# Performance work log

Hardware: AMD Instinct MI355X
Metric: run time of the kernel (lower is better)

Reference implementation:

```python
import jax, jax.numpy as jnp
import numpy as np
from itertools import combinations_with_replacement

KSIZE = 13  # 1 + 6*int(start_scale) with start_scale=2.0 (fixed at init)


def gaussian_kernel3d(scale):
    # torch: sigma = max(0.1, min(sigma, 10)); kernel detached (requires_grad=False)
    sigma = jnp.clip(jax.lax.stop_gradient(scale), 0.1, 10.0)
    k1 = jnp.arange(KSIZE, dtype=jnp.float32) - KSIZE // 2
    k1 = jnp.exp(-(k1 ** 2) / (2.0 * sigma ** 2))
    k3 = jnp.einsum('i,j,k->ijk', k1, k1, k1)
    return k3 / k3.sum()


def blur3d(vol, kernel):
    # replicate ('edge') padding then VALID conv, matching padding_mode='replicate'
    p = KSIZE // 2
    vp = jnp.pad(vol, ((0, 0), (0, 0), (p, p), (p, p), (p, p)), mode='edge')
    w = kernel[None, None]  # [O=1, I=1, kD, kH, kW]
    return jax.lax.conv_general_dilated(
        vp, w, window_strides=(1, 1, 1), padding='VALID',
        dimension_numbers=('NCDHW', 'OIDHW', 'NCDHW'))


def tgrad(f, axis):
    # torch.gradient: central diff interior, one-sided first-order at edges
    n = f.shape[axis]
    sl = lambda a, b: jax.lax.slice_in_dim(f, a, b, axis=axis)
    interior = (sl(2, n) - sl(0, n - 2)) * 0.5
    first = sl(1, 2) - sl(0, 1)
    last = sl(n - 1, n) - sl(n - 2, n - 1)
    return jnp.concatenate([first, interior, last], axis=axis)


def setup_inputs() -> dict:
    key = jax.random.key(0)
    kx, k1, k2, k3, k4 = jax.random.split(key, 5)
    B, D, H, W = 2, 128, 128, 128
    x = jax.random.normal(kx, (B, 1, D, H, W), dtype=jnp.float32)
    scale = jnp.asarray(2.0, dtype=jnp.float32)
    # Linear(7,10) and Linear(10,1), torch layout [out, in]
    lim1 = 1.0 / np.sqrt(7.0)
    lim2 = 1.0 / np.sqrt(10.0)
    W1 = jax.random.uniform(k1, (10, 7), jnp.float32, -lim1, lim1)
    b1 = jax.random.uniform(k2, (10,), jnp.float32, -lim1, lim1)
    W2 = jax.random.uniform(k3, (1, 10), jnp.float32, -lim2, lim2)
    b2 = jax.random.uniform(k4, (1,), jnp.float32, -lim2, lim2)
    return {'x': x, 'scale': scale, 'W1': W1, 'b1': b1, 'W2': W2, 'b2': b2}


def reference(x, scale, W1, b1, W2, b2):
    B = x.shape[0]
    D, H, W = x.shape[2], x.shape[3], x.shape[4]
    smoothed = blur3d(x, gaussian_kernel3d(scale))  # [B,1,D,H,W]
    axes = [2, 3, 4]
    g = [tgrad(smoothed, a) for a in axes]
    H_elems = [tgrad(g[a0 - 2], a1) for a0, a1 in combinations_with_replacement(axes, 2)]
    h = jnp.stack(H_elems)                      # [6,B,1,D,H,W]
    h = jnp.moveaxis(h, 0, -1)                  # [B,1,D,H,W,6]
    h = h.reshape(B, D * H * W, 6)              # flatten dims 1..4 (C=1)
    scale_col = jnp.broadcast_to(scale, (B, D * H * W, 1))
    feat = jnp.concatenate([h, scale_col], axis=2)  # [B,N,7]
    hid = jax.nn.relu(feat @ W1.T + b1)             # [B,N,10]
    out = jax.nn.sigmoid(hid @ W2.T + b2)           # [B,N,1]
    out = out.reshape(B, D, H, W, 1)
    return jnp.transpose(out, (0, 4, 1, 2, 3))      # [B,1,D,H,W]
```

## Files before the change

### kernel.cpp

```cpp
#include <hip/hip_runtime.h>
#include <math.h>

#define NVOX (2 * 128 * 128 * 128)
#define KS 13
#define KR 6
#define LROWS 44

__device__ __forceinline__ float4 LD4(const float* p) {
    return *reinterpret_cast<const float4*>(p);
}

__device__ __forceinline__ void make_weights(float scale, float* wv) {
    float sig = fminf(fmaxf(scale, 0.1f), 10.0f);
    float inv2s2 = -1.0f / (2.0f * sig * sig);
    float sum = 0.f;
#pragma unroll
    for (int t = 0; t < KS; ++t) {
        float d = (float)(t - KR);
        wv[t] = __expf(d * d * inv2s2);
        sum += wv[t];
    }
    float r = 1.0f / sum;
#pragma unroll
    for (int t = 0; t < KS; ++t) wv[t] *= r;
}

__global__ __launch_bounds__(256) void wh_blur_kernel(const float* __restrict__ in,
                                                      float* __restrict__ out,
                                                      const float* __restrict__ scale_p) {
    __shared__ float T[LROWS * 128];
    const int i = blockIdx.x;
    const int wid = ((i & 7) << 7) | (i >> 3);
    const int slice = wid >> 2;
    const int h0 = (wid & 3) << 5;
    const float* sp = in + (slice << 14);
    float* op = out + (slice << 14);

    float wv[KS];
    make_weights(scale_p[0], wv);

    for (int it = 0; it < 3; ++it) {
        int g = threadIdx.x + (it << 8);
        if (g < LROWS * 16) {
            int wseg = g & 15;
            int w0 = wseg << 3;
            int lr = g >> 4;
            int r = h0 - 6 + lr;
            r = r < 0 ? 0 : (r > 127 ? 127 : r);
            const float* rp = sp + (r << 7);

            float F[24];
            if (wseg >= 1 && wseg <= 14) {
#pragma unroll
                for (int i2 = 0; i2 < 6; ++i2) {
                    float4 q = LD4(rp + w0 - 8 + (i2 << 2));
                    F[4 * i2] = q.x; F[4 * i2 + 1] = q.y;
                    F[4 * i2 + 2] = q.z; F[4 * i2 + 3] = q.w;
                }
            } else if (wseg == 0) {
                float e = rp[0];
#pragma unroll
                for (int i2 = 0; i2 < 8; ++i2) F[i2] = e;
#pragma unroll
                for (int i2 = 0; i2 < 4; ++i2) {
                    float4 q = LD4(rp + (i2 << 2));
                    F[8 + 4 * i2] = q.x; F[9 + 4 * i2] = q.y;
                    F[10 + 4 * i2] = q.z; F[11 + 4 * i2] = q.w;
                }
            } else {
                float e = rp[127];
#pragma unroll
                for (int i2 = 0; i2 < 4; ++i2) {
                    float4 q = LD4(rp + 112 + (i2 << 2));
                    F[4 * i2] = q.x; F[4 * i2 + 1] = q.y;
                    F[4 * i2 + 2] = q.z; F[4 * i2 + 3] = q.w;
                }
#pragma unroll
                for (int i2 = 16; i2 < 24; ++i2) F[i2] = e;
            }

            float a[8];
#pragma unroll
            for (int k = 0; k < 8; ++k) a[k] = 0.f;
#pragma unroll
            for (int t = 0; t < KS; ++t) {
                float wt = wv[t];
#pragma unroll
                for (int k = 0; k < 8; ++k) a[k] = fmaf(wt, F[k + 2 + t], a[k]);
            }
            *reinterpret_cast<float4*>(&T[(lr << 7) + w0]) =
                make_float4(a[0], a[1], a[2], a[3]);
            *reinterpret_cast<float4*>(&T[(lr << 7) + w0 + 4]) =
                make_float4(a[4], a[5], a[6], a[7]);
        }
    }
    __syncthreads();

    {
        const int w0 = (threadIdx.x & 31) << 2;
        const int r0 = (threadIdx.x >> 5) << 2;

        float4 win[KS];
#pragma unroll
        for (int t = 0; t < KS; ++t) win[t] = LD4(&T[((r0 + t) << 7) + w0]);
#pragma unroll
        for (int s = 0; s < 4; ++s) {
            float4 acc = make_float4(0.f, 0.f, 0.f, 0.f);
#pragma unroll
            for (int t = 0; t < KS; ++t) {
                float4 v = win[(s + t) % KS];
                float wt = wv[t];
                acc.x = fmaf(wt, v.x, acc.x);
                acc.y = fmaf(wt, v.y, acc.y);
                acc.z = fmaf(wt, v.z, acc.z);
                acc.w = fmaf(wt, v.w, acc.w);
            }
            *reinterpret_cast<float4*>(op + ((h0 + r0 + s) << 7) + w0) = acc;
            int nl = r0 + s + 13;
            nl = nl > LROWS - 1 ? LROWS - 1 : nl;
            win[s % KS] = LD4(&T[(nl << 7) + w0]);
        }
    }
}

__global__ __launch_bounds__(256) void dblur_kernel(const float* __restrict__ in,
                                                    float* __restrict__ out,
                                                    const float* __restrict__ scale_p) {
    const int i = blockIdx.x;
    const int wid = ((i & 7) << 6) | (i >> 3);
    const int t0 = wid * 256 + threadIdx.x;
    const int w0 = (t0 & 31) << 2;
    const int h  = (t0 >> 5) & 127;
    const int d0 = ((t0 >> 12) & 15) << 3;
    const int b  = t0 >> 16;
    const int base = (b << 21) | (h << 7) | w0;

    float wv[KS];
    make_weights(scale_p[0], wv);

    float4 win[20];
#pragma unroll
    for (int t = 0; t < 20; ++t) {
        int r = d0 - 6 + t;
        r = r < 0 ? 0 : (r > 127 ? 127 : r);
        win[t] = LD4(in + base + (r << 14));
    }
#pragma unroll
    for (int s = 0; s < 8; ++s) {
        float4 acc = make_float4(0.f, 0.f, 0.f, 0.f);
#pragma unroll
        for (int t = 0; t < KS; ++t) {
            float4 v = win[s + t];
            float wt = wv[t];
            acc.x = fmaf(wt, v.x, acc.x);
            acc.y = fmaf(wt, v.y, acc.y);
            acc.z = fmaf(wt, v.z, acc.z);
            acc.w = fmaf(wt, v.w, acc.w);
        }
        *reinterpret_cast<float4*>(out + base + ((d0 + s) << 14)) = acc;
    }
}

__device__ __forceinline__ void lohi(int c, int& lo, int& hi, float& s) {
    lo = c > 0 ? c - 1 : 0;
    hi = c < 127 ? c + 1 : 127;
    s = 1.0f / (float)(hi - lo);
}

__device__ __forceinline__ int CH(int v) {
    return v < 0 ? 0 : (v > 127 ? 127 : v);
}

__global__ __launch_bounds__(256) void hess_mlp_kernel(const float* __restrict__ S,
                                const float* __restrict__ scale_p,
                                const float* __restrict__ W1, const float* __restrict__ b1,
                                const float* __restrict__ W2, const float* __restrict__ b2,
                                float* __restrict__ out) {
    const int i = blockIdx.x;
    const int wid = ((i & 7) << 7) | (i >> 3);
    const int t = wid * 256 + threadIdx.x;
    const int l = t & 31;
    const int w0 = l << 2;
    const int hb = ((t >> 5) & 31) << 2;
    const int d = (t >> 10) & 127;
    const int b = t >> 17;
    const int lane = threadIdx.x & 63;
    const bool l0 = (l == 0), l31 = (l == 31);

    int ld, hd; float sd; lohi(d, ld, hd, sd);
    int ti, tj; float s_hd, s_ld;
    lohi(hd, ti, tj, s_hd); lohi(ld, ti, tj, s_ld);
    const bool d_top = (d == 127), d_bot = (d == 0);
    const int dp2 = d > 125 ? 127 : d + 2;
    const int dm2 = d < 2 ? 0 : d - 2;

    float sw[4], s_hw[4], s_lw[4];
#pragma unroll
    for (int j = 0; j < 4; ++j) {
        int lw, hw; lohi(w0 + j, lw, hw, sw[j]);
        lohi(hw, ti, tj, s_hw[j]); lohi(lw, ti, tj, s_lw[j]);
    }

    const float scale = scale_p[0];
    float b1e[10];
#pragma unroll
    for (int u = 0; u < 10; ++u) b1e[u] = fmaf(scale, W1[u * 7 + 6], b1[u]);

    const float* base = S + (b << 21) + w0;
    auto RP = [&](int dd, int hh) { return base + (dd << 14) + (hh << 7); };
    float* obase = out + (b << 21) + (d << 14) + w0;

    float4 nd0 = LD4(RP(d, CH(hb - 2))), nd1 = LD4(RP(d, CH(hb - 1))),
           nd2 = LD4(RP(d, hb)),        nd3 = LD4(RP(d, hb + 1)),
           nd4 = LD4(RP(d, CH(hb + 2)));
    float4 pm0 = LD4(RP(ld, CH(hb - 1))), pm1 = LD4(RP(ld, hb)), pm2 = LD4(RP(ld, hb + 1));
    float4 pp0 = LD4(RP(hd, CH(hb - 1))), pp1 = LD4(RP(hd, hb)), pp2 = LD4(RP(hd, hb + 1));

#pragma unroll
    for (int s = 0; s < 4; ++s) {
        const int h = hb + s;
        const float4 qp = LD4(RP(dp2, h));
        const float4 qm = LD4(RP(dm2, h));

        int lh, hh; float sh; lohi(h, lh, hh, sh);
        float s_hh, s_lh; lohi(hh, ti, tj, s_hh); lohi(lh, ti, tj, s_lh);
        const bool h_top = (h == 127), h_bot = (h == 0);

        float c_lz = __shfl(nd2.z, lane - 1), c_lw = __shfl(nd2.w, lane - 1);
        float c_rx = __shfl(nd2.x, lane + 1), c_ry = __shfl(nd2.y, lane + 1);
        float r1_lw = __shfl(nd1.w, lane - 1), r1_rx = __shfl(nd1.x, lane + 1);
        float r3_lw = __shfl(nd3.w, lane - 1), r3_rx = __shfl(nd3.x, lane + 1);
        float pmlw = __shfl(pm1.w, lane - 1), pmrx = __shfl(pm1.x, lane + 1);
        float pplw = __shfl(pp1.w, lane - 1), pprx = __shfl(pp1.x, lane + 1);

        const float va[4]  = {nd2.x, nd2.y, nd2.z, nd2.w};
        const float n0a[4] = {nd0.x, nd0.y, nd0.z, nd0.w};
        const float n1a[4] = {nd1.x, nd1.y, nd1.z, nd1.w};
        const float n3a[4] = {nd3.x, nd3.y, nd3.z, nd3.w};
        const float n4a[4] = {nd4.x, nd4.y, nd4.z, nd4.w};
        const float pm0a[4] = {pm0.x, pm0.y, pm0.z, pm0.w};
        const float pm1a[4] = {pm1.x, pm1.y, pm1.z, pm1.w};
        const float pm2a[4] = {pm2.x, pm2.y, pm2.z, pm2.w};
        const float pp0a[4] = {pp0.x, pp0.y, pp0.z, pp0.w};
        const float pp1a[4] = {pp1.x, pp1.y, pp1.z, pp1.w};
        const float pp2a[4] = {pp2.x, pp2.y, pp2.z, pp2.w};
        const float qpa[4] = {qp.x, qp.y, qp.z, qp.w};
        const float qma[4] = {qm.x, qm.y, qm.z, qm.w};

        const float c_m1[4] = {l0 ? va[0] : c_lw, va[0], va[1], va[2]};
        const float c_p1[4] = {va[1], va[2], va[3], l31 ? va[3] : c_rx};
        const float c_m2[4] = {l0 ? va[0] : c_lz, l0 ? va[0] : c_lw, va[0], va[1]};
        const float c_p2[4] = {va[2], va[3], l31 ? va[3] : c_rx, l31 ? va[3] : c_ry};
        const float r1m[4] = {l0 ? n1a[0] : r1_lw, n1a[0], n1a[1], n1a[2]};
        const float r1p[4] = {n1a[1], n1a[2], n1a[3], l31 ? n1a[3] : r1_rx};
        const float r3m[4] = {l0 ? n3a[0] : r3_lw, n3a[0], n3a[1], n3a[2]};
        const float r3p[4] = {n3a[1], n3a[2], n3a[3], l31 ? n3a[3] : r3_rx};
        const float pmm[4] = {l0 ? pm1a[0] : pmlw, pm1a[0], pm1a[1], pm1a[2]};
        const float pmp[4] = {pm1a[1], pm1a[2], pm1a[3], l31 ? pm1a[3] : pmrx};
        const float ppm[4] = {l0 ? pp1a[0] : pplw, pp1a[0], pp1a[1], pp1a[2]};
        const float ppp[4] = {pp1a[1], pp1a[2], pp1a[3], l31 ? pp1a[3] : pprx};

        float ov[4];
#pragma unroll
        for (int j = 0; j < 4; ++j) {
            const float fDD = sd * (s_hd * (qpa[j] - (d_top ? pm1a[j] : va[j]))
                                  - s_ld * ((d_bot ? pp1a[j] : va[j]) - qma[j]));
            const float fHH = sh * (s_hh * (n4a[j] - (h_top ? n1a[j] : va[j]))
                                  - s_lh * ((h_bot ? n3a[j] : va[j]) - n0a[j]));
            const float fDH = sd * sh * ((pp2a[j] - pp0a[j]) - (pm2a[j] - pm0a[j]));
            const float fHW = sh * sw[j] * ((r3p[j] - r3m[j]) - (r1p[j] - r1m[j]));
            const float fDW = sd * sw[j] * ((ppp[j] - ppm[j]) - (pmp[j] - pmm[j]));
            const float Aw = (j == 3 && l31) ? c_m1[j] : va[j];
            const float Bw = (j == 0 && l0) ? c_p1[j] : va[j];
            const float fWW = sw[j] * (s_hw[j] * (c_p2[j] - Aw) - s_lw[j] * (Bw - c_m2[j]));

            const float ft[6] = {fDD, fDH, fDW, fHH, fHW, fWW};
            float o = b2[0];
#pragma unroll
            for (int u = 0; u < 10; ++u) {
                float a = b1e[u];
#pragma unroll
                for (int k = 0; k < 6; ++k) a = fmaf(ft[k], W1[u * 7 + k], a);
                a = fmaxf(a, 0.f);
                o = fmaf(a, W2[u], o);
            }
            float e = __expf(-o);
            ov[j] = __builtin_amdgcn_rcpf(1.0f + e);
        }
        *reinterpret_cast<float4*>(obase + (h << 7)) = make_float4(ov[0], ov[1], ov[2], ov[3]);

        nd0 = nd1; nd1 = nd2; nd2 = nd3; nd3 = nd4;
        nd4 = LD4(RP(d, CH(h + 3)));
        pm0 = pm1; pm1 = pm2; pm2 = LD4(RP(ld, CH(h + 2)));
        pp0 = pp1; pp1 = pp2; pp2 = LD4(RP(hd, CH(h + 2)));
    }
}

extern "C" void kernel_launch(void* const* d_in, const int* in_sizes, int n_in,
                              void* d_out, int out_size, void* d_ws, size_t ws_size,
                              hipStream_t stream) {
    const float* x     = (const float*)d_in[0];
    const float* scale = (const float*)d_in[1];
    const float* W1    = (const float*)d_in[2];
    const float* b1    = (const float*)d_in[3];
    const float* W2    = (const float*)d_in[4];
    const float* b2    = (const float*)d_in[5];
    float* out = (float*)d_out;

    float* ws0 = (float*)d_ws;
    float* ws1 = ws0 + NVOX;

    wh_blur_kernel<<<2 * 128 * 4, 256, 0, stream>>>(x, ws1, scale);
    dblur_kernel<<<NVOX / 32 / 256, 256, 0, stream>>>(ws1, ws0, scale);
    hess_mlp_kernel<<<NVOX / 16 / 256, 256, 0, stream>>>(ws0, scale, W1, b1, W2, b2, out);
}
```

Measured before the change: 44.45 us.

## Fuse depth blur into Hessian-MLP kernel via shared-memory tile with halo recompute

```diff
diff --git a/kernel.cpp b/kernel.cpp
--- a/kernel.cpp
+++ b/kernel.cpp
@@ -23,6 +23,16 @@
     float r = 1.0f / sum;
 #pragma unroll
     for (int t = 0; t < KS; ++t) wv[t] *= r;
+}
+
+__device__ __forceinline__ int CH(int v) {
+    return v < 0 ? 0 : (v > 127 ? 127 : v);
+}
+
+__device__ __forceinline__ void lohi(int c, int& lo, int& hi, float& s) {
+    lo = c > 0 ? c - 1 : 0;
+    hi = c < 127 ? c + 1 : 127;
+    s = 1.0f / (float)(hi - lo);
 }
 
 __global__ __launch_bounds__(256) void wh_blur_kernel(const float* __restrict__ in,
@@ -123,76 +133,64 @@
     }
 }
 
-__global__ __launch_bounds__(256) void dblur_kernel(const float* __restrict__ in,
-                                                    float* __restrict__ out,
-                                                    const float* __restrict__ scale_p) {
-    const int i = blockIdx.x;
-    const int wid = ((i & 7) << 6) | (i >> 3);
-    const int t0 = wid * 256 + threadIdx.x;
-    const int w0 = (t0 & 31) << 2;
-    const int h  = (t0 >> 5) & 127;
-    const int d0 = ((t0 >> 12) & 15) << 3;
-    const int b  = t0 >> 16;
-    const int base = (b << 21) | (h << 7) | w0;
-
-    float wv[KS];
-    make_weights(scale_p[0], wv);
-
-    float4 win[20];
-#pragma unroll
-    for (int t = 0; t < 20; ++t) {
-        int r = d0 - 6 + t;
-        r = r < 0 ? 0 : (r > 127 ? 127 : r);
-        win[t] = LD4(in + base + (r << 14));
-    }
-#pragma unroll
-    for (int s = 0; s < 8; ++s) {
-        float4 acc = make_float4(0.f, 0.f, 0.f, 0.f);
-#pragma unroll
-        for (int t = 0; t < KS; ++t) {
-            float4 v = win[s + t];
-            float wt = wv[t];
-            acc.x = fmaf(wt, v.x, acc.x);
-            acc.y = fmaf(wt, v.y, acc.y);
-            acc.z = fmaf(wt, v.z, acc.z);
-            acc.w = fmaf(wt, v.w, acc.w);
-        }
-        *reinterpret_cast<float4*>(out + base + ((d0 + s) << 14)) = acc;
-    }
-}
-
-__device__ __forceinline__ void lohi(int c, int& lo, int& hi, float& s) {
-    lo = c > 0 ? c - 1 : 0;
-    hi = c < 127 ? c + 1 : 127;
-    s = 1.0f / (float)(hi - lo);
-}
-
-__device__ __forceinline__ int CH(int v) {
-    return v < 0 ? 0 : (v > 127 ? 127 : v);
-}
-
-__global__ __launch_bounds__(256) void hess_mlp_kernel(const float* __restrict__ S,
+__global__ __launch_bounds__(256) void dhess_kernel(const float* __restrict__ ws1,
                                 const float* __restrict__ scale_p,
                                 const float* __restrict__ W1, const float* __restrict__ b1,
                                 const float* __restrict__ W2, const float* __restrict__ b2,
                                 float* __restrict__ out) {
+    __shared__ float S[8][12][128];
     const int i = blockIdx.x;
     const int wid = ((i & 7) << 7) | (i >> 3);
-    const int t = wid * 256 + threadIdx.x;
-    const int l = t & 31;
+    const int b  = wid >> 9;
+    const int d0 = ((wid >> 4) & 31) << 2;
+    const int hb = (wid & 15) << 3;
+
+    float wv[KS];
+    make_weights(scale_p[0], wv);
+    const float* wbase = ws1 + (b << 21);
+
+    for (int it = 0; it < 2; ++it) {
+        int col = (it << 8) + threadIdx.x;
+        if (col < 384) {
+            int r = col >> 5;
+            int w0 = (col & 31) << 2;
+            int gr = CH(hb - 2 + r);
+            const float* cb = wbase + (gr << 7) + w0;
+            float4 win[20];
+#pragma unroll
+            for (int k = 0; k < 20; ++k) {
+                int g = d0 - 8 + k;
+                g = g < 0 ? 0 : (g > 127 ? 127 : g);
+                win[k] = LD4(cb + (g << 14));
+            }
+#pragma unroll
+            for (int p = 0; p < 8; ++p) {
+                float4 acc = make_float4(0.f, 0.f, 0.f, 0.f);
+#pragma unroll
+                for (int t = 0; t < KS; ++t) {
+                    float4 v = win[p + t];
+                    float wt = wv[t];
+                    acc.x = fmaf(wt, v.x, acc.x);
+                    acc.y = fmaf(wt, v.y, acc.y);
+                    acc.z = fmaf(wt, v.z, acc.z);
+                    acc.w = fmaf(wt, v.w, acc.w);
+                }
+                *reinterpret_cast<float4*>(&S[p][r][w0]) = acc;
+            }
+        }
+    }
+    __syncthreads();
+
+    const int l  = threadIdx.x & 31;
+    const int hj = threadIdx.x >> 5;
     const int w0 = l << 2;
-    const int hb = ((t >> 5) & 31) << 2;
-    const int d = (t >> 10) & 127;
-    const int b = t >> 17;
-    const int lane = threadIdx.x & 63;
+    const int h  = hb + hj;
     const bool l0 = (l == 0), l31 = (l == 31);
 
-    int ld, hd; float sd; lohi(d, ld, hd, sd);
-    int ti, tj; float s_hd, s_ld;
-    lohi(hd, ti, tj, s_hd); lohi(ld, ti, tj, s_ld);
-    const bool d_top = (d == 127), d_bot = (d == 0);
-    const int dp2 = d > 125 ? 127 : d + 2;
-    const int dm2 = d < 2 ? 0 : d - 2;
+    int ti, tj;
+    int lh, hh; float sh; lohi(h, lh, hh, sh);
+    float s_hh, s_lh; lohi(hh, ti, tj, s_hh); lohi(lh, ti, tj, s_lh);
+    const bool h_top = (h == 127), h_bot = (h == 0);
 
     float sw[4], s_hw[4], s_lw[4];
 #pragma unroll
@@ -205,77 +203,85 @@
     float b1e[10];
 #pragma unroll
     for (int u = 0; u < 10; ++u) b1e[u] = fmaf(scale, W1[u * 7 + 6], b1[u]);
-
-    const float* base = S + (b << 21) + w0;
-    auto RP = [&](int dd, int hh) { return base + (dd << 14) + (hh << 7); };
-    float* obase = out + (b << 21) + (d << 14) + w0;
-
-    float4 nd0 = LD4(RP(d, CH(hb - 2))), nd1 = LD4(RP(d, CH(hb - 1))),
-           nd2 = LD4(RP(d, hb)),        nd3 = LD4(RP(d, hb + 1)),
-           nd4 = LD4(RP(d, CH(hb + 2)));
-    float4 pm0 = LD4(RP(ld, CH(hb - 1))), pm1 = LD4(RP(ld, hb)), pm2 = LD4(RP(ld, hb + 1));
-    float4 pp0 = LD4(RP(hd, CH(hb - 1))), pp1 = LD4(RP(hd, hb)), pp2 = LD4(RP(hd, hb + 1));
-
-#pragma unroll
-    for (int s = 0; s < 4; ++s) {
-        const int h = hb + s;
-        const float4 qp = LD4(RP(dp2, h));
-        const float4 qm = LD4(RP(dm2, h));
-
-        int lh, hh; float sh; lohi(h, lh, hh, sh);
-        float s_hh, s_lh; lohi(hh, ti, tj, s_hh); lohi(lh, ti, tj, s_lh);
-        const bool h_top = (h == 127), h_bot = (h == 0);
-
-        float c_lz = __shfl(nd2.z, lane - 1), c_lw = __shfl(nd2.w, lane - 1);
-        float c_rx = __shfl(nd2.x, lane + 1), c_ry = __shfl(nd2.y, lane + 1);
-        float r1_lw = __shfl(nd1.w, lane - 1), r1_rx = __shfl(nd1.x, lane + 1);
-        float r3_lw = __shfl(nd3.w, lane - 1), r3_rx = __shfl(nd3.x, lane + 1);
-        float pmlw = __shfl(pm1.w, lane - 1), pmrx = __shfl(pm1.x, lane + 1);
-        float pplw = __shfl(pp1.w, lane - 1), pprx = __shfl(pp1.x, lane + 1);
-
-        const float va[4]  = {nd2.x, nd2.y, nd2.z, nd2.w};
-        const float n0a[4] = {nd0.x, nd0.y, nd0.z, nd0.w};
-        const float n1a[4] = {nd1.x, nd1.y, nd1.z, nd1.w};
-        const float n3a[4] = {nd3.x, nd3.y, nd3.z, nd3.w};
-        const float n4a[4] = {nd4.x, nd4.y, nd4.z, nd4.w};
-        const float pm0a[4] = {pm0.x, pm0.y, pm0.z, pm0.w};
-        const float pm1a[4] = {pm1.x, pm1.y, pm1.z, pm1.w};
-        const float pm2a[4] = {pm2.x, pm2.y, pm2.z, pm2.w};
-        const float pp0a[4] = {pp0.x, pp0.y, pp0.z, pp0.w};
-        const float pp1a[4] = {pp1.x, pp1.y, pp1.z, pp1.w};
-        const float pp2a[4] = {pp2.x, pp2.y, pp2.z, pp2.w};
-        const float qpa[4] = {qp.x, qp.y, qp.z, qp.w};
-        const float qma[4] = {qm.x, qm.y, qm.z, qm.w};
-
-        const float c_m1[4] = {l0 ? va[0] : c_lw, va[0], va[1], va[2]};
-        const float c_p1[4] = {va[1], va[2], va[3], l31 ? va[3] : c_rx};
-        const float c_m2[4] = {l0 ? va[0] : c_lz, l0 ? va[0] : c_lw, va[0], va[1]};
-        const float c_p2[4] = {va[2], va[3], l31 ? va[3] : c_rx, l31 ? va[3] : c_ry};
-        const float r1m[4] = {l0 ? n1a[0] : r1_lw, n1a[0], n1a[1], n1a[2]};
-        const float r1p[4] = {n1a[1], n1a[2], n1a[3], l31 ? n1a[3] : r1_rx};
-        const float r3m[4] = {l0 ? n3a[0] : r3_lw, n3a[0], n3a[1], n3a[2]};
-        const float r3p[4] = {n3a[1], n3a[2], n3a[3], l31 ? n3a[3] : r3_rx};
-        const float pmm[4] = {l0 ? pm1a[0] : pmlw, pm1a[0], pm1a[1], pm1a[2]};
-        const float pmp[4] = {pm1a[1], pm1a[2], pm1a[3], l31 ? pm1a[3] : pmrx};
-        const float ppm[4] = {l0 ? pp1a[0] : pplw, pp1a[0], pp1a[1], pp1a[2]};
-        const float ppp[4] = {pp1a[1], pp1a[2], pp1a[3], l31 ? pp1a[3] : pprx};
+    const float b2s = b2[0];
+
+    const int lr0  = hj + 2;
+    const int lrm1 = CH(h - 1) - hb + 2;
+    const int lrm2 = CH(h - 2) - hb + 2;
+    const int lrp1 = CH(h + 1) - hb + 2;
+    const int lrp2 = CH(h + 2) - hb + 2;
+
+    const int wm2 = CH(w0 - 2), wm1 = CH(w0 - 1);
+    const int wp4 = CH(w0 + 4), wp5 = CH(w0 + 5);
+
+    float* obase = out + (b << 21) + (h << 7) + w0;
+
+#pragma unroll
+    for (int dj = 0; dj < 4; ++dj) {
+        const int d = d0 + dj;
+        int ld, hd; float sd; lohi(d, ld, hd, sd);
+        float s_hd, s_ld; lohi(hd, ti, tj, s_hd); lohi(ld, ti, tj, s_ld);
+        const bool d_top = (d == 127), d_bot = (d == 0);
+        const int lpd   = dj + 2;
+        const int lpld  = ld - d0 + 2;
+        const int lphd  = hd - d0 + 2;
+        const int lpdp2 = CH(d + 2) - d0 + 2;
+        const int lpdm2 = CH(d - 2) - d0 + 2;
+
+        const float* rv = &S[lpd][lr0][0];
+        float4 vq = LD4(&rv[w0]);
+        const float va8[8] = {rv[wm2], rv[wm1], vq.x, vq.y, vq.z, vq.w, rv[wp4], rv[wp5]};
+
+        const float* rn1 = &S[lpd][lrm1][0];
+        float4 n1q = LD4(&rn1[w0]);
+        const float n1_6[6] = {rn1[wm1], n1q.x, n1q.y, n1q.z, n1q.w, rn1[wp4]};
+
+        const float* rn3 = &S[lpd][lrp1][0];
+        float4 n3q = LD4(&rn3[w0]);
+        const float n3_6[6] = {rn3[wm1], n3q.x, n3q.y, n3q.z, n3q.w, rn3[wp4]};
+
+        const float* rpm = &S[lpld][lr0][0];
+        float4 pm1q = LD4(&rpm[w0]);
+        const float pm1_6[6] = {rpm[wm1], pm1q.x, pm1q.y, pm1q.z, pm1q.w, rpm[wp4]};
+
+        const float* rpp = &S[lphd][lr0][0];
+        float4 pp1q = LD4(&rpp[w0]);
+        const float pp1_6[6] = {rpp[wm1], pp1q.x, pp1q.y, pp1q.z, pp1q.w, rpp[wp4]};
+
+        float4 n0q  = LD4(&S[lpd][lrm2][w0]);
+        float4 n4q  = LD4(&S[lpd][lrp2][w0]);
+        float4 pm0q = LD4(&S[lpld][lrm1][w0]);
+        float4 pm2q = LD4(&S[lpld][lrp1][w0]);
+        float4 pp0q = LD4(&S[lphd][lrm1][w0]);
+        float4 pp2q = LD4(&S[lphd][lrp1][w0]);
+        float4 qpq  = LD4(&S[lpdp2][lr0][w0]);
+        float4 qmq  = LD4(&S[lpdm2][lr0][w0]);
+
+        const float n0f[4]  = {n0q.x, n0q.y, n0q.z, n0q.w};
+        const float n4f[4]  = {n4q.x, n4q.y, n4q.z, n4q.w};
+        const float pm0f[4] = {pm0q.x, pm0q.y, pm0q.z, pm0q.w};
+        const float pm2f[4] = {pm2q.x, pm2q.y, pm2q.z, pm2q.w};
+        const float pp0f[4] = {pp0q.x, pp0q.y, pp0q.z, pp0q.w};
+        const float pp2f[4] = {pp2q.x, pp2q.y, pp2q.z, pp2q.w};
+        const float qpf[4]  = {qpq.x, qpq.y, qpq.z, qpq.w};
+        const float qmf[4]  = {qmq.x, qmq.y, qmq.z, qmq.w};
 
         float ov[4];
 #pragma unroll
         for (int j = 0; j < 4; ++j) {
-            const float fDD = sd * (s_hd * (qpa[j] - (d_top ? pm1a[j] : va[j]))
-                                  - s_ld * ((d_bot ? pp1a[j] : va[j]) - qma[j]));
-            const float fHH = sh * (s_hh * (n4a[j] - (h_top ? n1a[j] : va[j]))
-                                  - s_lh * ((h_bot ? n3a[j] : va[j]) - n0a[j]));
-            const float fDH = sd * sh * ((pp2a[j] - pp0a[j]) - (pm2a[j] - pm0a[j]));
-            const float fHW = sh * sw[j] * ((r3p[j] - r3m[j]) - (r1p[j] - r1m[j]));
-            const float fDW = sd * sw[j] * ((ppp[j] - ppm[j]) - (pmp[j] - pmm[j]));
-            const float Aw = (j == 3 && l31) ? c_m1[j] : va[j];
-            const float Bw = (j == 0 && l0) ? c_p1[j] : va[j];
-            const float fWW = sw[j] * (s_hw[j] * (c_p2[j] - Aw) - s_lw[j] * (Bw - c_m2[j]));
+            const float fDD = sd * (s_hd * (qpf[j] - (d_top ? pm1_6[j + 1] : va8[j + 2]))
+                                  - s_ld * ((d_bot ? pp1_6[j + 1] : va8[j + 2]) - qmf[j]));
+            const float fHH = sh * (s_hh * (n4f[j] - (h_top ? n1_6[j + 1] : va8[j + 2]))
+                                  - s_lh * ((h_bot ? n3_6[j + 1] : va8[j + 2]) - n0f[j]));
+            const float fDH = sd * sh * ((pp2f[j] - pp0f[j]) - (pm2f[j] - pm0f[j]));
+            const float fHW = sh * sw[j] * ((n3_6[j + 2] - n3_6[j]) - (n1_6[j + 2] - n1_6[j]));
+            const float fDW = sd * sw[j] * ((pp1_6[j + 2] - pp1_6[j]) - (pm1_6[j + 2] - pm1_6[j]));
+            const float Aw = (j == 3 && l31) ? va8[j + 1] : va8[j + 2];
+            const float Bw = (j == 0 && l0) ? va8[j + 3] : va8[j + 2];
+            const float fWW = sw[j] * (s_hw[j] * (va8[j + 4] - Aw) - s_lw[j] * (Bw - va8[j]));
 
             const float ft[6] = {fDD, fDH, fDW, fHH, fHW, fWW};
-            float o = b2[0];
+            float o = b2s;
 #pragma unroll
             for (int u = 0; u < 10; ++u) {
                 float a = b1e[u];
@@ -287,12 +293,7 @@
             float e = __expf(-o);
             ov[j] = __builtin_amdgcn_rcpf(1.0f + e);
         }
-        *reinterpret_cast<float4*>(obase + (h << 7)) = make_float4(ov[0], ov[1], ov[2], ov[3]);
-
-        nd0 = nd1; nd1 = nd2; nd2 = nd3; nd3 = nd4;
-        nd4 = LD4(RP(d, CH(h + 3)));
-        pm0 = pm1; pm1 = pm2; pm2 = LD4(RP(ld, CH(h + 2)));
-        pp0 = pp1; pp1 = pp2; pp2 = LD4(RP(hd, CH(h + 2)));
+        *reinterpret_cast<float4*>(obase + (d << 14)) = make_float4(ov[0], ov[1], ov[2], ov[3]);
     }
 }
 
@@ -307,10 +308,8 @@
     const float* b2    = (const float*)d_in[5];
     float* out = (float*)d_out;
 
-    float* ws0 = (float*)d_ws;
-    float* ws1 = ws0 + NVOX;
+    float* ws1 = (float*)d_ws;
 
     wh_blur_kernel<<<2 * 128 * 4, 256, 0, stream>>>(x, ws1, scale);
-    dblur_kernel<<<NVOX / 32 / 256, 256, 0, stream>>>(ws1, ws0, scale);
-    hess_mlp_kernel<<<NVOX / 16 / 256, 256, 0, stream>>>(ws0, scale, W1, b1, W2, b2, out);
-}
+    dhess_kernel<<<2 * 32 * 16, 256, 0, stream>>>(ws1, scale, W1, b1, W2, b2, out);
+}
```

Result: slower. 47.54 us (+6.9%).

## Stage depth-blur halo in shared memory to cut redundant global reads

Applied to the files above, without the earlier changes.

```diff
diff --git a/kernel.cpp b/kernel.cpp
--- a/kernel.cpp
+++ b/kernel.cpp
@@ -23,6 +23,16 @@
     float r = 1.0f / sum;
 #pragma unroll
     for (int t = 0; t < KS; ++t) wv[t] *= r;
+}
+
+__device__ __forceinline__ int CH(int v) {
+    return v < 0 ? 0 : (v > 127 ? 127 : v);
+}
+
+__device__ __forceinline__ void lohi(int c, int& lo, int& hi, float& s) {
+    lo = c > 0 ? c - 1 : 0;
+    hi = c < 127 ? c + 1 : 127;
+    s = 1.0f / (float)(hi - lo);
 }
 
 __global__ __launch_bounds__(256) void wh_blur_kernel(const float* __restrict__ in,
@@ -126,49 +136,53 @@
 __global__ __launch_bounds__(256) void dblur_kernel(const float* __restrict__ in,
                                                     float* __restrict__ out,
                                                     const float* __restrict__ scale_p) {
+    __shared__ float P[76][128];
     const int i = blockIdx.x;
     const int wid = ((i & 7) << 6) | (i >> 3);
-    const int t0 = wid * 256 + threadIdx.x;
-    const int w0 = (t0 & 31) << 2;
-    const int h  = (t0 >> 5) & 127;
-    const int d0 = ((t0 >> 12) & 15) << 3;
-    const int b  = t0 >> 16;
-    const int base = (b << 21) | (h << 7) | w0;
+    const int b     = wid >> 8;
+    const int dhalf = (wid >> 7) & 1;
+    const int h     = wid & 127;
+    const int d0    = dhalf << 6;
+    const int tid   = threadIdx.x;
 
     float wv[KS];
     make_weights(scale_p[0], wv);
 
-    float4 win[20];
-#pragma unroll
-    for (int t = 0; t < 20; ++t) {
-        int r = d0 - 6 + t;
-        r = r < 0 ? 0 : (r > 127 ? 127 : r);
-        win[t] = LD4(in + base + (r << 14));
-    }
+    const float* rbase = in + (b << 21) + (h << 7);
+#pragma unroll
+    for (int k = 0; k < 10; ++k) {
+        int idx = (k << 8) + tid;
+        if (idx < 76 * 32) {
+            int p = idx >> 5;
+            int c = (idx & 31) << 2;
+            int g = CH(d0 - 6 + p);
+            *reinterpret_cast<float4*>(&P[p][c]) = LD4(rbase + (g << 14) + c);
+        }
+    }
+    __syncthreads();
+
+    const int dg = tid >> 5;
+    const int w0 = (tid & 31) << 2;
+    float* obase = out + (b << 21) + (h << 7) + w0;
+
+    float4 wreg[20];
+#pragma unroll
+    for (int t = 0; t < 20; ++t) wreg[t] = LD4(&P[(dg << 3) + t][w0]);
+
 #pragma unroll
     for (int s = 0; s < 8; ++s) {
         float4 acc = make_float4(0.f, 0.f, 0.f, 0.f);
 #pragma unroll
         for (int t = 0; t < KS; ++t) {
-            float4 v = win[s + t];
+            float4 v = wreg[s + t];
             float wt = wv[t];
             acc.x = fmaf(wt, v.x, acc.x);
             acc.y = fmaf(wt, v.y, acc.y);
             acc.z = fmaf(wt, v.z, acc.z);
             acc.w = fmaf(wt, v.w, acc.w);
         }
-        *reinterpret_cast<float4*>(out + base + ((d0 + s) << 14)) = acc;
-    }
-}
-
-__device__ __forceinline__ void lohi(int c, int& lo, int& hi, float& s) {
-    lo = c > 0 ? c - 1 : 0;
-    hi = c < 127 ? c + 1 : 127;
-    s = 1.0f / (float)(hi - lo);
-}
-
-__device__ __forceinline__ int CH(int v) {
-    return v < 0 ? 0 : (v > 127 ? 127 : v);
+        *reinterpret_cast<float4*>(obase + ((d0 + (dg << 3) + s) << 14)) = acc;
+    }
 }
 
 __global__ __launch_bounds__(256) void hess_mlp_kernel(const float* __restrict__ S,
@@ -311,6 +325,6 @@
     float* ws1 = ws0 + NVOX;
 
     wh_blur_kernel<<<2 * 128 * 4, 256, 0, stream>>>(x, ws1, scale);
-    dblur_kernel<<<NVOX / 32 / 256, 256, 0, stream>>>(ws1, ws0, scale);
+    dblur_kernel<<<512, 256, 0, stream>>>(ws1, ws0, scale);
     hess_mlp_kernel<<<NVOX / 16 / 256, 256, 0, stream>>>(ws0, scale, W1, b1, W2, b2, out);
 }
```

Result: no change. 45.05 us (+1.4%).
